# Optimization experiments

Hardware: AMD Instinct MI355X
Metric: run time of the kernel (lower is better)

## Reference

```python
import jax, jax.numpy as jnp
import numpy as np

DIM = 1152
NUM_HEADS = 16
HEAD_DIM = DIM // NUM_HEADS
EPS = 1e-6
B, N, M = 4, 4096, 512


def setup_inputs() -> dict:
    key = jax.random.key(0)
    ks = jax.random.split(key, 12)
    s = 0.02
    return {
        "x": jax.random.normal(ks[0], (B, N, DIM), dtype=jnp.float32),
        "cond": jax.random.normal(ks[1], (B, M, DIM), dtype=jnp.float32),
        "kv_seqlen": jax.random.randint(ks[2], (B,), 1, M + 1, dtype=jnp.int32),
        "q_w": jax.random.normal(ks[3], (DIM, DIM), dtype=jnp.float32) * s,
        "q_b": jnp.zeros((DIM,), jnp.float32),
        "kv_w": jax.random.normal(ks[4], (DIM, 2 * DIM), dtype=jnp.float32) * s,
        "kv_b": jnp.zeros((2 * DIM,), jnp.float32),
        "proj_w": jax.random.normal(ks[5], (DIM, DIM), dtype=jnp.float32) * s,
        "proj_b": jnp.zeros((DIM,), jnp.float32),
        "qn_w": jnp.ones((HEAD_DIM,), jnp.float32),
        "kn_w": jnp.ones((HEAD_DIM,), jnp.float32),
    }


def _rmsnorm_fp32(t, w):
    # RMSNorm computed in fp32 over head_dim, then cast back
    t32 = t.astype(jnp.float32)
    inv = jax.lax.rsqrt(jnp.mean(t32 * t32, axis=-1, keepdims=True) + EPS)
    return ((t32 * inv) * w.astype(jnp.float32)).astype(t.dtype)


def reference(x, cond, kv_seqlen, q_w, q_b, kv_w, kv_b, proj_w, proj_b, qn_w, kn_w):
    b, n, c = x.shape
    out_dtype = x.dtype
    q = (x @ q_w + q_b).reshape(b, n, NUM_HEADS, HEAD_DIM)           # [B,N,H,D]
    kv = (cond @ kv_w + kv_b).reshape(b, -1, 2, NUM_HEADS, HEAD_DIM)
    k, v = kv[:, :, 0], kv[:, :, 1]                                   # [B,M,H,D]
    q = _rmsnorm_fp32(q, qn_w)
    k = _rmsnorm_fp32(k, kn_w)
    # original casts to bf16 for the attention kernel when out_dtype is fp32
    q16, k16, v16 = q.astype(jnp.bfloat16), k.astype(jnp.bfloat16), v.astype(jnp.bfloat16)
    scale = 1.0 / np.sqrt(HEAD_DIM)
    scores = jnp.einsum("bnhd,bmhd->bhnm", q16, k16,
                        preferred_element_type=jnp.float32) * scale   # [B,H,N,M] fp32
    m = cond.shape[1]
    valid = (jnp.arange(m)[None, :] < kv_seqlen[:, None])             # [B,M] ragged kv mask
    scores = jnp.where(valid[:, None, None, :], scores, -jnp.inf)
    probs = jax.nn.softmax(scores, axis=-1).astype(jnp.bfloat16)
    out = jnp.einsum("bhnm,bmhd->bnhd", probs, v16).reshape(b, n, c)
    out = out.astype(out_dtype)
    return out @ proj_w + proj_b
```

## Files before the change

### kernel.cpp

```cpp
#include <hip/hip_runtime.h>
#include <math.h>

typedef unsigned short ushort_t;
typedef __attribute__((ext_vector_type(4))) float floatx4;
typedef __attribute__((ext_vector_type(8))) short bf16x8;

#define DIMC 1152
#define NHEADS 16
#define HDIM 72

__device__ __forceinline__ ushort_t f2bf(float f) {
  unsigned u = __float_as_uint(f);
  u += 0x7FFFu + ((u >> 16) & 1u);
  return (ushort_t)(u >> 16);
}
__device__ __forceinline__ float bf2f(ushort_t s) {
  return __uint_as_float(((unsigned)s) << 16);
}

__device__ __forceinline__ void gload_lds16(const ushort_t* g, ushort_t* l) {
  __builtin_amdgcn_global_load_lds(
      (const __attribute__((address_space(1))) unsigned int*)(const void*)g,
      (__attribute__((address_space(3))) unsigned int*)(void*)l, 16, 0, 0);
}

__device__ __forceinline__ bf16x8 load_bf16x8(const ushort_t* p) {
  union { bf16x8 v; uint4 u; } t;
  t.u = *(const uint4*)p;
  return t.v;
}

__global__ void prep_kernel(const float* __restrict__ x, ushort_t* __restrict__ x16,
                            const float* __restrict__ cond, ushort_t* __restrict__ cond16,
                            const float* __restrict__ q_w, ushort_t* __restrict__ qwT,
                            const float* __restrict__ kv_w, ushort_t* __restrict__ kvwT,
                            const float* __restrict__ proj_w, ushort_t* __restrict__ pwT) {
  __shared__ ushort_t tile[64 * 80];
  int blk = blockIdx.x;
  int tid = threadIdx.x;

  if (blk < 10368) {
    const float* src; ushort_t* dst; int i;
    if (blk < 9216) { src = x; dst = x16; i = blk * 256 + tid; }
    else            { src = cond; dst = cond16; i = (blk - 9216) * 256 + tid; }
    float4 f0 = ((const float4*)src)[2 * (size_t)i];
    float4 f1 = ((const float4*)src)[2 * (size_t)i + 1];
    union { ushort_t s[8]; uint4 u; } t;
    t.s[0] = f2bf(f0.x); t.s[1] = f2bf(f0.y); t.s[2] = f2bf(f0.z); t.s[3] = f2bf(f0.w);
    t.s[4] = f2bf(f1.x); t.s[5] = f2bf(f1.y); t.s[6] = f2bf(f1.z); t.s[7] = f2bf(f1.w);
    ((uint4*)dst)[i] = t.u;
    return;
  }

  const float* W; ushort_t* Wt; int N, idx;
  if (blk < 10692)      { W = q_w;    Wt = qwT;  N = 1152; idx = blk - 10368; }
  else if (blk < 11340) { W = kv_w;   Wt = kvwT; N = 2304; idx = blk - 10692; }
  else                  { W = proj_w; Wt = pwT;  N = 1152; idx = blk - 11340; }
  const int K = 1152;
  int k0 = (idx % 18) * 64, n0 = (idx / 18) * 64;

  int kl = tid >> 4, n4 = tid & 15;
  for (int rr = 0; rr < 4; rr++) {
    int k = kl + rr * 16;
    float4 f = *(const float4*)(W + (size_t)(k0 + k) * N + n0 + n4 * 4);
    tile[(n4 * 4 + 0) * 80 + k] = f2bf(f.x);
    tile[(n4 * 4 + 1) * 80 + k] = f2bf(f.y);
    tile[(n4 * 4 + 2) * 80 + k] = f2bf(f.z);
    tile[(n4 * 4 + 3) * 80 + k] = f2bf(f.w);
  }
  __syncthreads();
  int nl = tid >> 2, kq = tid & 3;
  uint4 v0 = *(const uint4*)(tile + nl * 80 + kq * 16);
  uint4 v1 = *(const uint4*)(tile + nl * 80 + kq * 16 + 8);
  *(uint4*)(Wt + (size_t)(n0 + nl) * K + k0 + kq * 16) = v0;
  *(uint4*)(Wt + (size_t)(n0 + nl) * K + k0 + kq * 16 + 8) = v1;
}

template <bool OUT_F32>
__global__ __launch_bounds__(256, 2) void gemm128_kernel(
    const ushort_t* __restrict__ A0, const ushort_t* __restrict__ Bt0,
    const float* __restrict__ bias0, void* __restrict__ C0,
    int NTn0, int Ncols0,
    const ushort_t* __restrict__ A1, const ushort_t* __restrict__ Bt1,
    const float* __restrict__ bias1, void* __restrict__ C1,
    int NTn1, int Ncols1,
    int nblk0, int Kdim) {
  __shared__ ushort_t S[32768];

  int lin = blockIdx.x;
  int cpx = gridDim.x >> 3;
  int wg = (lin & 7) * cpx + (lin >> 3);

  const ushort_t* Aseg; const ushort_t* Bseg;
  const float* bias; void* Cptr; int NTn, Ncols;
  if (wg < nblk0) {
    Aseg = A0; Bseg = Bt0; bias = bias0; Cptr = C0; NTn = NTn0; Ncols = Ncols0;
  } else {
    wg -= nblk0;
    Aseg = A1; Bseg = Bt1; bias = bias1; Cptr = C1; NTn = NTn1; Ncols = Ncols1;
  }
  int mt = wg / NTn, nt = wg % NTn;
  int m0 = mt * 128, n0 = nt * 128;

  int tid = threadIdx.x;
  int wid = tid >> 6, lane = tid & 63, quad = lane >> 4, l16 = lane & 15;
  int wr = wid >> 1, wc = wid & 1;
  const int qoff = (quad * 8) ^ ((l16 & 8) << 1);

  const int srow = tid >> 2;
  const int scol = ((tid & 3) * 8) ^ ((tid & 32) ? 16 : 0);
  const ushort_t* Abase = Aseg + (size_t)m0 * Kdim;
  const ushort_t* Bbase = Bseg + (size_t)n0 * Kdim;

  auto stageA = [&](int t, int ks) {
    const ushort_t* src = Abase + (size_t)srow * Kdim + t * 64 + ks * 32 + scol;
    ushort_t* dst = S + (t & 1) * 16384 + ks * 4096 + (tid >> 6) * 512;
    gload_lds16(src, dst);
    gload_lds16(src + (size_t)64 * Kdim, dst + 2048);
  };
  auto stageB = [&](int t, int ks) {
    const ushort_t* src = Bbase + (size_t)srow * Kdim + t * 64 + ks * 32 + scol;
    ushort_t* dst = S + (t & 1) * 16384 + 8192 + ks * 4096 + (tid >> 6) * 512;
    gload_lds16(src, dst);
    gload_lds16(src + (size_t)64 * Kdim, dst + 2048);
  };

  floatx4 zero = {0.f, 0.f, 0.f, 0.f};
  floatx4 acc[4][4];
#pragma unroll
  for (int i = 0; i < 4; i++)
#pragma unroll
    for (int j = 0; j < 4; j++) acc[i][j] = zero;

  int NT = Kdim >> 6;

  stageA(0, 0); stageB(0, 0);
  stageA(0, 1); stageB(0, 1);
  asm volatile("s_waitcnt vmcnt(4)" ::: "memory");
  __builtin_amdgcn_s_barrier();

  for (int t = 0; t < NT; ++t) {
    const int abase = (t & 1) * 16384;
    const int arow = (wr * 64 + l16) * 32 + qoff;
    const int brow = (wc * 64 + l16) * 32 + qoff;

#pragma unroll
    for (int ks = 0; ks < 2; ++ks) {
      const int ab = abase + ks * 4096;
      const int bb = abase + 8192 + ks * 4096;
      bf16x8 af[4], bfr[4];
#pragma unroll
      for (int mf = 0; mf < 4; mf++)
        af[mf] = *(const bf16x8*)(S + ab + arow + mf * 512);
#pragma unroll
      for (int c = 0; c < 4; c++)
        bfr[c] = *(const bf16x8*)(S + bb + brow + c * 512);
      if (t + 1 < NT) { stageA(t + 1, ks); stageB(t + 1, ks); }
      __builtin_amdgcn_s_barrier();
      asm volatile("s_waitcnt lgkmcnt(0)" ::: "memory");
      __builtin_amdgcn_sched_barrier(0);
      __builtin_amdgcn_s_setprio(1);
#pragma unroll
      for (int c = 0; c < 4; c++)
#pragma unroll
        for (int mf = 0; mf < 4; mf++)
          acc[mf][c] = __builtin_amdgcn_mfma_f32_16x16x32_bf16(af[mf], bfr[c], acc[mf][c], 0, 0, 0);
      __builtin_amdgcn_s_setprio(0);
      if (t + 1 < NT)
        asm volatile("s_waitcnt vmcnt(4)" ::: "memory");
      else
        asm volatile("s_waitcnt vmcnt(0)" ::: "memory");
      __builtin_amdgcn_s_barrier();
    }
  }

  float bv[4];
#pragma unroll
  for (int c = 0; c < 4; c++) bv[c] = bias[n0 + wc * 64 + c * 16 + l16];
#pragma unroll
  for (int mf = 0; mf < 4; mf++)
#pragma unroll
    for (int c = 0; c < 4; c++)
#pragma unroll
      for (int r = 0; r < 4; r++) {
        int row = m0 + wr * 64 + mf * 16 + quad * 4 + r;
        int col = n0 + wc * 64 + c * 16 + l16;
        float v = acc[mf][c][r] + bv[c];
        if constexpr (OUT_F32)
          ((float*)Cptr)[(size_t)row * Ncols + col] = v;
        else
          ((ushort_t*)Cptr)[(size_t)row * Ncols + col] = f2bf(v);
      }
}

__global__ void rmsvt_kernel(ushort_t* __restrict__ kv16,
                             const float* __restrict__ kn_w,
                             ushort_t* __restrict__ vT) {
  __shared__ ushort_t tile[64 * 84];
  int blk = blockIdx.x;
  int tid = threadIdx.x;

  if (blk < 8192) {
    int gw = blk * 4 + (tid >> 6);
    int lane = tid & 63;
    int row = gw >> 4, h = gw & 15;
    ushort_t* base = kv16 + (size_t)row * 2304 + h * HDIM;
    float v0 = bf2f(base[lane]);
    float v1 = (lane < 8) ? bf2f(base[64 + lane]) : 0.f;
    float ss = v0 * v0 + v1 * v1;
    for (int off = 1; off < 64; off <<= 1) ss += __shfl_xor(ss, off);
    float inv = rsqrtf(ss / 72.0f + 1e-6f);
    base[lane] = f2bf(v0 * inv * kn_w[lane]);
    if (lane < 8) base[64 + lane] = f2bf(v1 * inv * kn_w[64 + lane]);
    return;
  }

  int idx = blk - 8192;
  int m0 = (idx & 7) * 64, h = (idx >> 3) & 15, b = idx >> 7;
  int row = tid >> 2, sl = tid & 3;
  const ushort_t* src =
      kv16 + (size_t)(b * 512 + m0 + row) * 2304 + DIMC + h * HDIM;
#pragma unroll
  for (int k = 0; k < 5; k++) {
    int s = sl + 4 * k;
    if (s < 18) {
      uint2 v = *(const uint2*)(src + s * 4);
      *(uint2*)(tile + row * 84 + s * 4) = v;
    }
  }
  __syncthreads();
  size_t dbase = (size_t)((b * 16 + h) * 80) * 512 + m0;
#pragma unroll
  for (int it = 0; it < 5; it++) {
    int i2 = it * 256 + tid;
    int d = i2 >> 4, mseg = i2 & 15;
    union { ushort_t s[4]; uint2 u; } pk;
    if (d < HDIM) {
      pk.s[0] = tile[(mseg * 4 + 0) * 84 + d];
      pk.s[1] = tile[(mseg * 4 + 1) * 84 + d];
      pk.s[2] = tile[(mseg * 4 + 2) * 84 + d];
      pk.s[3] = tile[(mseg * 4 + 3) * 84 + d];
    } else {
      ushort_t f = (d == HDIM) ? (ushort_t)0x3F80 : (ushort_t)0;
      pk.s[0] = pk.s[1] = pk.s[2] = pk.s[3] = f;
    }
    *(uint2*)(vT + dbase + (size_t)d * 512 + mseg * 4) = pk.u;
  }
}

__global__ __launch_bounds__(256, 4) void attn_kernel(
    const ushort_t* __restrict__ q16, const ushort_t* __restrict__ kv16,
    const ushort_t* __restrict__ vT, const int* __restrict__ seqlens,
    const float* __restrict__ qn_w, ushort_t* __restrict__ att) {
  __shared__ ushort_t KV[22 * 512];
  __shared__ __align__(16) unsigned Ps[4][32 * 32];
  int lin = blockIdx.x;
  int xcd = lin & 7, slot = lin >> 3;
  int bh = xcd * 8 + (slot >> 5);
  int b = bh >> 4, h = bh & 15;
  int n0 = (slot & 31) * 128;
  int tid = threadIdx.x, wid = tid >> 6, lane = tid & 63;
  int quad = lane >> 4, l16 = lane & 15;
  int seqlen = seqlens[b];
  const float qscale = 0.11785113019775793f * 1.44269504088896f;

  unsigned* Pw = &Ps[wid][0];
  const int xorm = (l16 & 7) << 2;

  bf16x8 qf[2][3];
  float ssq[2] = {0.f, 0.f};
  for (int rb = 0; rb < 2; rb++)
    for (int ks = 0; ks < 3; ks++) {
      if (ks == 2 && quad > 0) {
        qf[rb][ks] = (bf16x8){0, 0, 0, 0, 0, 0, 0, 0};
      } else {
        size_t off = ((size_t)(b * 4096 + n0 + wid * 32 + rb * 16 + l16)) * DIMC +
                     h * HDIM + ks * 32 + quad * 8;
        qf[rb][ks] = load_bf16x8(q16 + off);
        union { bf16x8 v; ushort_t s[8]; } e;
        e.v = qf[rb][ks];
        for (int j = 0; j < 8; j++) {
          float xv = bf2f(e.s[j]);
          ssq[rb] += xv * xv;
        }
      }
    }
  for (int rb = 0; rb < 2; rb++) {
    ssq[rb] += __shfl_xor(ssq[rb], 16);
    ssq[rb] += __shfl_xor(ssq[rb], 32);
  }
  for (int rb = 0; rb < 2; rb++) {
    float inv = rsqrtf(ssq[rb] / 72.0f + 1e-6f) * qscale;
    for (int ks = 0; ks < 3; ks++) {
      if (ks == 2 && quad > 0) continue;
      float4 w0 = *(const float4*)(qn_w + ks * 32 + quad * 8);
      float4 w1 = *(const float4*)(qn_w + ks * 32 + quad * 8 + 4);
      union { bf16x8 v; ushort_t s[8]; } e;
      e.v = qf[rb][ks];
      e.s[0] = f2bf(bf2f(e.s[0]) * inv * w0.x);
      e.s[1] = f2bf(bf2f(e.s[1]) * inv * w0.y);
      e.s[2] = f2bf(bf2f(e.s[2]) * inv * w0.z);
      e.s[3] = f2bf(bf2f(e.s[3]) * inv * w0.w);
      e.s[4] = f2bf(bf2f(e.s[4]) * inv * w1.x);
      e.s[5] = f2bf(bf2f(e.s[5]) * inv * w1.y);
      e.s[6] = f2bf(bf2f(e.s[6]) * inv * w1.z);
      e.s[7] = f2bf(bf2f(e.s[7]) * inv * w1.w);
      qf[rb][ks] = e.v;
    }
  }

  floatx4 zero = {0.f, 0.f, 0.f, 0.f};
  floatx4 of[2][5];
  for (int rb = 0; rb < 2; rb++)
    for (int nf = 0; nf < 5; nf++) of[rb][nf] = zero;

  const size_t kvrow = (size_t)b * 512;
  const size_t vbase = (size_t)((b * 16 + h) * 80) * 512;

  int ntiles = (seqlen + 63) >> 6;
  for (int mt = 0; mt < ntiles; mt++) {
    int m0 = mt * 64;

    __syncthreads();
    for (int id = wid; id < 22; id += 4) {
      const ushort_t* src;
      if (id < 12) {
        int c = (id * 11) >> 5;
        int ks = id - c * 3;
        src = kv16 + (size_t)(kvrow + m0 + c * 16 + l16) * 2304 + h * HDIM +
              ks * 32 + quad * 8;
      } else {
        int v = id - 12;
        int nf = v >> 1, ks = v & 1;
        src = vT + (vbase + (size_t)(nf * 16 + l16) * 512) + m0 + ks * 32 + quad * 8;
      }
      gload_lds16(src, KV + id * 512);
    }
    __syncthreads();

    floatx4 sf[2][4];
    for (int rb = 0; rb < 2; rb++)
      for (int c = 0; c < 4; c++) sf[rb][c] = zero;
    for (int c = 0; c < 4; c++)
      for (int ks = 0; ks < 3; ks++) {
        bf16x8 kf = *(const bf16x8*)(KV + (c * 3 + ks) * 512 + lane * 8);
        for (int rb = 0; rb < 2; rb++)
          sf[rb][c] = __builtin_amdgcn_mfma_f32_16x16x32_bf16(kf, qf[rb][ks], sf[rb][c], 0, 0, 0);
      }

    bool partial = (m0 + 64) > seqlen;
    for (int rb = 0; rb < 2; rb++) {
      unsigned* prow = Pw + (rb * 16 + l16) * 32;
      for (int c = 0; c < 4; c++) {
        float p0 = __builtin_amdgcn_exp2f(sf[rb][c][0]);
        float p1 = __builtin_amdgcn_exp2f(sf[rb][c][1]);
        float p2 = __builtin_amdgcn_exp2f(sf[rb][c][2]);
        float p3 = __builtin_amdgcn_exp2f(sf[rb][c][3]);
        if (partial) {
          int kabs = m0 + c * 16 + quad * 4;
          p0 = (kabs < seqlen) ? p0 : 0.f;
          p1 = (kabs + 1 < seqlen) ? p1 : 0.f;
          p2 = (kabs + 2 < seqlen) ? p2 : 0.f;
          p3 = (kabs + 3 < seqlen) ? p3 : 0.f;
        }
        unsigned w0, w1;
        asm("v_cvt_pk_bf16_f32 %0, %1, %2" : "=v"(w0) : "v"(p0), "v"(p1));
        asm("v_cvt_pk_bf16_f32 %0, %1, %2" : "=v"(w1) : "v"(p2), "v"(p3));
        uint2 pw2; pw2.x = w0; pw2.y = w1;
        *(uint2*)(prow + ((8 * c + 2 * quad) ^ xorm)) = pw2;
      }
    }

    for (int ks = 0; ks < 2; ks++) {
      bf16x8 pf[2];
      for (int rb = 0; rb < 2; rb++) {
        const unsigned* prow = Pw + (rb * 16 + l16) * 32;
        pf[rb] = *(const bf16x8*)(prow + ((ks * 16 + quad * 4) ^ xorm));
      }
      for (int nf = 0; nf < 5; nf++) {
        bf16x8 vf = *(const bf16x8*)(KV + (12 + nf * 2 + ks) * 512 + lane * 8);
        for (int rb = 0; rb < 2; rb++)
          of[rb][nf] = __builtin_amdgcn_mfma_f32_16x16x32_bf16(pf[rb], vf, of[rb][nf], 0, 0, 0);
      }
    }
  }

  for (int rb = 0; rb < 2; rb++) {
    float invl[4];
    for (int r = 0; r < 4; r++) {
      float lsum = __shfl(of[rb][4][r], (lane & 48) | 8);
      invl[r] = 1.0f / lsum;
    }
    for (int nf = 0; nf < 5; nf++) {
      int d = nf * 16 + l16;
      if (d < HDIM) {
        for (int r = 0; r < 4; r++) {
          size_t o = ((size_t)(b * 4096 + n0 + wid * 32 + rb * 16 + quad * 4 + r)) * DIMC +
                     h * HDIM + d;
          att[o] = f2bf(of[rb][nf][r] * invl[r]);
        }
      }
    }
  }
}

extern "C" void kernel_launch(void* const* d_in, const int* in_sizes, int n_in,
                              void* d_out, int out_size, void* d_ws, size_t ws_size,
                              hipStream_t stream) {
  const float* x      = (const float*)d_in[0];
  const float* cond   = (const float*)d_in[1];
  const int*   seqlen = (const int*)d_in[2];
  const float* q_w    = (const float*)d_in[3];
  const float* q_b    = (const float*)d_in[4];
  const float* kv_w   = (const float*)d_in[5];
  const float* kv_b   = (const float*)d_in[6];
  const float* proj_w = (const float*)d_in[7];
  const float* proj_b = (const float*)d_in[8];
  const float* qn_w   = (const float*)d_in[9];
  const float* kn_w   = (const float*)d_in[10];
  float* out = (float*)d_out;

  char* ws = (char*)d_ws;
  size_t o = 0;
  ushort_t* qwT    = (ushort_t*)(ws + o); o += (size_t)1152 * 1152 * 2;
  ushort_t* kvwT   = (ushort_t*)(ws + o); o += (size_t)2304 * 1152 * 2;
  ushort_t* pwT    = (ushort_t*)(ws + o); o += (size_t)1152 * 1152 * 2;
  ushort_t* q16    = (ushort_t*)(ws + o); o += (size_t)16384 * 1152 * 2;
  ushort_t* kv16   = (ushort_t*)(ws + o); o += (size_t)2048 * 2304 * 2;
  ushort_t* vT     = (ushort_t*)(ws + o); o += (size_t)64 * 80 * 512 * 2;
  ushort_t* att    = (ushort_t*)(ws + o); o += (size_t)16384 * 1152 * 2;
  ushort_t* x16    = (ushort_t*)(ws + o); o += (size_t)16384 * 1152 * 2;
  ushort_t* cond16 = (ushort_t*)(ws + o); o += (size_t)2048 * 1152 * 2;

  dim3 blk(256);

  prep_kernel<<<dim3(11664), blk, 0, stream>>>(
      x, x16, cond, cond16, q_w, qwT, kv_w, kvwT, proj_w, pwT);

  gemm128_kernel<false><<<dim3(1152 + 288), blk, 0, stream>>>(
      x16, qwT, q_b, q16, 9, 1152,
      cond16, kvwT, kv_b, kv16, 18, 2304,
      1152, 1152);

  rmsvt_kernel<<<dim3(8192 + 512), blk, 0, stream>>>(kv16, kn_w, vT);

  attn_kernel<<<dim3(2048), blk, 0, stream>>>(q16, kv16, vT, seqlen, qn_w, att);

  gemm128_kernel<true><<<dim3(1152), blk, 0, stream>>>(
      att, pwT, proj_b, out, 9, 1152,
      att, pwT, proj_b, out, 9, 1152,
      1152, 1152);
}
```

Measured before the change: 370.0 us.

## Double-buffer KV tiles in attention with async LDS prefetch and remap heads

The attention kernel now keeps two LDS buffers for the K/V tiles. Each wave issues global-to-LDS loads for the next tile before computing on the current one, and waits with explicit vmcnt and barriers instead of two __syncthreads around a blocking load. Load addresses are precomputed once per thread and advanced by a fixed stride each tile. The block-to-(batch, head) mapping is also changed so that consecutive XCDs take different heads. The doubled LDS and the launch bound lowered from 4 to 2 cut resident blocks per CU in exchange for overlapping memory latency with MFMA work.

After: 380.8 us. 1.03x slower.

```diff
diff --git a/kernel.cpp b/kernel.cpp
--- a/kernel.cpp
+++ b/kernel.cpp
@@ -248,15 +248,15 @@
   }
 }
 
-__global__ __launch_bounds__(256, 4) void attn_kernel(
+__global__ __launch_bounds__(256, 2) void attn_kernel(
     const ushort_t* __restrict__ q16, const ushort_t* __restrict__ kv16,
     const ushort_t* __restrict__ vT, const int* __restrict__ seqlens,
     const float* __restrict__ qn_w, ushort_t* __restrict__ att) {
-  __shared__ ushort_t KV[22 * 512];
+  __shared__ ushort_t KV[2 * 22 * 512];
   __shared__ __align__(16) unsigned Ps[4][32 * 32];
   int lin = blockIdx.x;
   int xcd = lin & 7, slot = lin >> 3;
-  int bh = xcd * 8 + (slot >> 5);
+  int bh = (slot >> 5) * 8 + xcd;
   int b = bh >> 4, h = bh & 15;
   int n0 = (slot & 31) * 128;
   int tid = threadIdx.x, wid = tid >> 6, lane = tid & 63;
@@ -266,6 +266,28 @@
 
   unsigned* Pw = &Ps[wid][0];
   const int xorm = (l16 & 7) << 2;
+
+  const size_t kvrow = (size_t)b * 512;
+  const size_t vbase = (size_t)((b * 16 + h) * 80) * 512;
+
+  const ushort_t* sp[6];
+  int sst[6], sdst[6];
+#pragma unroll
+  for (int j = 0; j < 6; j++) {
+    int id = wid * 6 + j;
+    int rid = (id < 22) ? id : id - 22;
+    if (rid < 12) {
+      int c = (rid * 11) >> 5, ks = rid - c * 3;
+      sp[j] = kv16 + (size_t)(kvrow + c * 16 + l16) * 2304 + h * HDIM +
+              ks * 32 + quad * 8;
+      sst[j] = 64 * 2304;
+    } else {
+      int v = rid - 12, nf = v >> 1, ks = v & 1;
+      sp[j] = vT + vbase + (size_t)(nf * 16 + l16) * 512 + ks * 32 + quad * 8;
+      sst[j] = 64;
+    }
+    sdst[j] = rid * 512 + lane * 8;
+  }
 
   bf16x8 qf[2][3];
   float ssq[2] = {0.f, 0.f};
@@ -314,36 +336,38 @@
   for (int rb = 0; rb < 2; rb++)
     for (int nf = 0; nf < 5; nf++) of[rb][nf] = zero;
 
-  const size_t kvrow = (size_t)b * 512;
-  const size_t vbase = (size_t)((b * 16 + h) * 80) * 512;
-
   int ntiles = (seqlen + 63) >> 6;
+
+#pragma unroll
+  for (int j = 0; j < 6; j++) {
+    gload_lds16(sp[j], KV + sdst[j]);
+    sp[j] += sst[j];
+  }
+
   for (int mt = 0; mt < ntiles; mt++) {
+    const int cur = (mt & 1) * 11264;
+    if (mt + 1 < ntiles) {
+      const int nxt = ((mt + 1) & 1) * 11264;
+#pragma unroll
+      for (int j = 0; j < 6; j++) {
+        gload_lds16(sp[j], KV + nxt + sdst[j]);
+        sp[j] += sst[j];
+      }
+      asm volatile("s_waitcnt vmcnt(6)" ::: "memory");
+    } else {
+      asm volatile("s_waitcnt vmcnt(0)" ::: "memory");
+    }
+    __builtin_amdgcn_s_barrier();
+    __builtin_amdgcn_sched_barrier(0);
+
     int m0 = mt * 64;
-
-    __syncthreads();
-    for (int id = wid; id < 22; id += 4) {
-      const ushort_t* src;
-      if (id < 12) {
-        int c = (id * 11) >> 5;
-        int ks = id - c * 3;
-        src = kv16 + (size_t)(kvrow + m0 + c * 16 + l16) * 2304 + h * HDIM +
-              ks * 32 + quad * 8;
-      } else {
-        int v = id - 12;
-        int nf = v >> 1, ks = v & 1;
-        src = vT + (vbase + (size_t)(nf * 16 + l16) * 512) + m0 + ks * 32 + quad * 8;
-      }
-      gload_lds16(src, KV + id * 512);
-    }
-    __syncthreads();
 
     floatx4 sf[2][4];
     for (int rb = 0; rb < 2; rb++)
       for (int c = 0; c < 4; c++) sf[rb][c] = zero;
     for (int c = 0; c < 4; c++)
       for (int ks = 0; ks < 3; ks++) {
-        bf16x8 kf = *(const bf16x8*)(KV + (c * 3 + ks) * 512 + lane * 8);
+        bf16x8 kf = *(const bf16x8*)(KV + cur + (c * 3 + ks) * 512 + lane * 8);
         for (int rb = 0; rb < 2; rb++)
           sf[rb][c] = __builtin_amdgcn_mfma_f32_16x16x32_bf16(kf, qf[rb][ks], sf[rb][c], 0, 0, 0);
       }
@@ -378,11 +402,14 @@
         pf[rb] = *(const bf16x8*)(prow + ((ks * 16 + quad * 4) ^ xorm));
       }
       for (int nf = 0; nf < 5; nf++) {
-        bf16x8 vf = *(const bf16x8*)(KV + (12 + nf * 2 + ks) * 512 + lane * 8);
+        bf16x8 vf = *(const bf16x8*)(KV + cur + (12 + nf * 2 + ks) * 512 + lane * 8);
         for (int rb = 0; rb < 2; rb++)
           of[rb][nf] = __builtin_amdgcn_mfma_f32_16x16x32_bf16(pf[rb], vf, of[rb][nf], 0, 0, 0);
       }
     }
+
+    asm volatile("s_waitcnt lgkmcnt(0)" ::: "memory");
+    __builtin_amdgcn_s_barrier();
   }
 
   for (int rb = 0; rb < 2; rb++) {
```
